# Optimization experiments

Measured on AMD Instinct MI355X. Metric: run time of the kernel, lower is better.

## Reference

```python
import jax, jax.numpy as jnp
import numpy as np

D_MODEL = 512; N_LAYERS = 6; D_STATE = 128; EXPAND = 2
D_INNER = EXPAND * D_MODEL          # 1024
HEADDIM = 64; NHEADS = D_INNER // HEADDIM  # 16
D_CONV = 4
CONV_DIM = D_INNER + 2 * D_STATE    # 1280 (x, B, C share the causal conv)
D_IN_PROJ = 2 * D_INNER + 2 * D_STATE + NHEADS  # 2320 (z, xBC, dt)
CHUNK = 128
B_SZ = 2; SEQ = 4096


def setup_inputs() -> dict:
    key = jax.random.key(0)
    ks = jax.random.split(key, 8)
    return {
        "x": jax.random.normal(ks[0], (B_SZ, SEQ, D_MODEL), jnp.float32),
        "in_proj_w": jax.random.normal(ks[1], (N_LAYERS, D_IN_PROJ, D_MODEL), jnp.float32) * 0.02,
        "conv_w": jax.random.normal(ks[2], (N_LAYERS, CONV_DIM, 1, D_CONV), jnp.float32) * 0.1,
        "conv_b": jnp.zeros((N_LAYERS, CONV_DIM), jnp.float32),
        "dt_bias": jax.random.normal(ks[3], (N_LAYERS, NHEADS), jnp.float32) * 0.5,
        "A_log": jnp.log(jax.random.uniform(ks[4], (N_LAYERS, NHEADS), jnp.float32, 1.0, 16.0)),
        "D": jax.random.normal(ks[5], (N_LAYERS, NHEADS), jnp.float32) * 0.1 + 1.0,
        "rms_w": jnp.ones((N_LAYERS, D_INNER), jnp.float32),
        "out_proj_w": jax.random.normal(ks[6], (N_LAYERS, D_MODEL, D_INNER), jnp.float32) * 0.02,
        "ln_w": jnp.ones((N_LAYERS, D_MODEL), jnp.float32),
        "ln_b": jnp.zeros((N_LAYERS, D_MODEL), jnp.float32),
        "fln_w": jnp.ones((D_MODEL,), jnp.float32),
        "fln_b": jnp.zeros((D_MODEL,), jnp.float32),
    }


def _layernorm(x, w, b, eps=1e-5):
    mu = jnp.mean(x, -1, keepdims=True)
    xc = x - mu
    var = jnp.mean(xc * xc, -1, keepdims=True)
    return xc * jax.lax.rsqrt(var + eps) * w + b


def _segsum(a):
    # a: (..., T) -> (..., T, T); S[i,j] = sum_{j<k<=i} a[k] for i>=j else -inf
    T = a.shape[-1]
    c = jnp.cumsum(a, -1)
    s = c[..., :, None] - c[..., None, :]
    return jnp.where(jnp.tril(jnp.ones((T, T), bool)), s, -jnp.inf)


def _ssd(xdt, Adt, Bm, Cm):
    # Chunked Mamba-2 SSD (math-identical to h_t = exp(dt*A) h_{t-1} + dt*B_t x_t; y_t = C_t h_t)
    # xdt: (b,l,h,p) = x*dt; Adt: (b,l,h) = dt*A; Bm, Cm: (b,l,n) (ngroups=1)
    b, l, h, p = xdt.shape
    n = Bm.shape[-1]
    c = l // CHUNK
    X = xdt.reshape(b, c, CHUNK, h, p)
    A = Adt.reshape(b, c, CHUNK, h).transpose(0, 3, 1, 2)  # (b,h,c,q)
    Bc = Bm.reshape(b, c, CHUNK, n)
    Cc = Cm.reshape(b, c, CHUNK, n)
    A_cs = jnp.cumsum(A, -1)                                # (b,h,c,q)
    Lm = jnp.exp(_segsum(A))                                # (b,h,c,q,q) intra-chunk decays
    Y_diag = jnp.einsum('bcqn,bcsn,bhcqs,bcshp->bcqhp', Cc, Bc, Lm, X)
    decay_states = jnp.exp(A_cs[..., -1:] - A_cs)           # (b,h,c,q)
    states = jnp.einsum('bcqn,bhcq,bcqhp->bchpn', Bc, decay_states, X)  # chunk end states
    A_last = A_cs[..., -1]                                  # (b,h,c)
    dc = jnp.exp(_segsum(jnp.pad(A_last, ((0, 0), (0, 0), (1, 0)))))    # (b,h,c+1,c+1)
    states = jnp.concatenate([jnp.zeros_like(states[:, :1]), states], axis=1)  # (b,c+1,h,p,n)
    new_states = jnp.einsum('bhzc,bchpn->bzhpn', dc, states)
    init_states = new_states[:, :-1]                        # state entering each chunk
    Y_off = jnp.einsum('bcqn,bchpn,bhcq->bcqhp', Cc, init_states, jnp.exp(A_cs))
    return (Y_diag + Y_off).reshape(b, l, h, p)


def _mamba2(u, Wi, cw, cb, dtb, Alog, Dh, rw, Wo):
    b, l, _ = u.shape
    zxbcdt = u @ Wi.T                                      # (b,l,2320)
    z = zxbcdt[..., :D_INNER]
    xBC = zxbcdt[..., D_INNER:D_INNER + CONV_DIM]
    dt = jax.nn.softplus(zxbcdt[..., D_INNER + CONV_DIM:] + dtb)  # (b,l,h)
    # causal depthwise conv (kernel 4)
    xp = jnp.pad(xBC, ((0, 0), (D_CONV - 1, 0), (0, 0))).transpose(0, 2, 1)
    conv = jax.lax.conv_general_dilated(xp, cw, (1,), 'VALID', feature_group_count=CONV_DIM)
    xBC = jax.nn.silu(conv.transpose(0, 2, 1) + cb)
    xh = xBC[..., :D_INNER].reshape(b, l, NHEADS, HEADDIM)
    Bm = xBC[..., D_INNER:D_INNER + D_STATE]
    Cm = xBC[..., D_INNER + D_STATE:]
    A = -jnp.exp(Alog)                                     # (h,)
    y = _ssd(xh * dt[..., None], dt * A, Bm, Cm)
    y = y + Dh[None, None, :, None] * xh                   # D skip
    y = y.reshape(b, l, D_INNER)
    yz = y * jax.nn.silu(z)                                # gated RMSNorm
    y = yz * jax.lax.rsqrt(jnp.mean(yz * yz, -1, keepdims=True) + 1e-5) * rw
    return y @ Wo.T


def reference(x, in_proj_w, conv_w, conv_b, dt_bias, A_log, D, rms_w, out_proj_w, ln_w, ln_b, fln_w, fln_b):
    h = x
    for i in range(N_LAYERS):
        res = h
        hn = _layernorm(h, ln_w[i], ln_b[i])
        h = _mamba2(hn, in_proj_w[i], conv_w[i], conv_b[i], dt_bias[i], A_log[i], D[i], rms_w[i], out_proj_w[i]) + res
    return _layernorm(h, fln_w, fln_b)
```

## Files before the change

### kernel.cpp

```cpp
#include <hip/hip_runtime.h>
#include <hip/hip_bf16.h>
#include <math.h>

#define BQ 2
#define SEQL 4096
#define DM 512
#define DIN 1024
#define DSTATE 128
#define NH 16
#define HD 64
#define DCONV 4
#define CONVDIM 1280
#define DINPROJ 2320
#define CHUNKL 128
#define NCHUNK 32
#define ROWS (BQ*SEQL)
#define NPAD 2304

typedef __attribute__((ext_vector_type(8))) short short8;
typedef __attribute__((ext_vector_type(4))) short short4v;
typedef __attribute__((ext_vector_type(4))) float f32x4;

__device__ __forceinline__ short bfs(float f) {
  __hip_bfloat16 h = __float2bfloat16(f);
  short s; __builtin_memcpy(&s, &h, 2); return s;
}
__device__ __forceinline__ float sbf(short s) {
  __hip_bfloat16 h; __builtin_memcpy(&h, &s, 2); return __bfloat162float(h);
}

__global__ __launch_bounds__(256) void ln_kernel(const float* __restrict__ in, const float* __restrict__ w,
                                                 const float* __restrict__ b, float* __restrict__ out,
                                                 __hip_bfloat16* __restrict__ outb) {
  int r = blockIdx.x;
  const float* x = in + (size_t)r * DM;
  float v[2];
  float s = 0.f, ss = 0.f;
  for (int i = 0; i < 2; i++) { v[i] = x[threadIdx.x + i*256]; s += v[i]; ss += v[i]*v[i]; }
  for (int o = 32; o > 0; o >>= 1) { s += __shfl_down(s, o); ss += __shfl_down(ss, o); }
  __shared__ float red[2][4];
  int lane = threadIdx.x & 63, wv = threadIdx.x >> 6;
  if (lane == 0) { red[0][wv] = s; red[1][wv] = ss; }
  __syncthreads();
  s  = red[0][0] + red[0][1] + red[0][2] + red[0][3];
  ss = red[1][0] + red[1][1] + red[1][2] + red[1][3];
  float mu = s * (1.f/DM);
  float var = ss * (1.f/DM) - mu*mu;
  float rstd = rsqrtf(var + 1e-5f);
  for (int i = 0; i < 2; i++) {
    int idx = threadIdx.x + i*256;
    float val = (v[i]-mu)*rstd*w[idx] + b[idx];
    out[(size_t)r*DM + idx] = val;
    if (outb) outb[(size_t)r*DM + idx] = __float2bfloat16(val);
  }
}

__global__ __launch_bounds__(256) void ln_dt_kernel(const float* __restrict__ in, const float* __restrict__ w,
                                                    const float* __restrict__ b, const float* __restrict__ Wi,
                                                    const float* __restrict__ dtb,
                                                    __hip_bfloat16* __restrict__ outb, float* __restrict__ dtout) {
  int r = blockIdx.x;
  const float* x = in + (size_t)r * DM;
  __shared__ float sh[512];
  __shared__ float red2[2][4];
  __shared__ float red[16][17];
  int t = threadIdx.x;
  float v[2];
  float s = 0.f, ss = 0.f;
  for (int i = 0; i < 2; i++) { v[i] = x[t + i*256]; s += v[i]; ss += v[i]*v[i]; }
  for (int o = 32; o > 0; o >>= 1) { s += __shfl_down(s, o); ss += __shfl_down(ss, o); }
  int lane = t & 63, wv = t >> 6;
  if (lane == 0) { red2[0][wv] = s; red2[1][wv] = ss; }
  __syncthreads();
  s  = red2[0][0] + red2[0][1] + red2[0][2] + red2[0][3];
  ss = red2[1][0] + red2[1][1] + red2[1][2] + red2[1][3];
  float mu = s * (1.f/DM);
  float var = ss * (1.f/DM) - mu*mu;
  float rstd = rsqrtf(var + 1e-5f);
  for (int i = 0; i < 2; i++) {
    int idx = t + i*256;
    float val = (v[i]-mu)*rstd*w[idx] + b[idx];
    sh[idx] = val;
    outb[(size_t)r*DM + idx] = __float2bfloat16(val);
  }
  __syncthreads();
  int j = t >> 4, seg = t & 15;
  const float* wrow = Wi + (size_t)(2304 + j)*DM + seg*32;
  float p = 0.f;
  #pragma unroll
  for (int k = 0; k < 32; k++) p += sh[seg*32 + k] * wrow[k];
  red[j][seg] = p;
  __syncthreads();
  if (t < 16) {
    float vv = 0.f;
    for (int sgi = 0; sgi < 16; sgi++) vv += red[t][sgi];
    vv += dtb[t];
    dtout[r*NH + t] = (vv > 20.f) ? vv : log1pf(__expf(vv));
  }
}

__global__ __launch_bounds__(256) void cvt_wi(const float* __restrict__ Wi, __hip_bfloat16* __restrict__ out) {
  int idx = blockIdx.x*256 + threadIdx.x;
  int l = idx / (NPAD*DM);
  int r = idx - l*(NPAD*DM);
  int n = r >> 9, k = r & 511;
  out[idx] = __float2bfloat16(Wi[(size_t)l*DINPROJ*DM + (size_t)n*DM + k]);
}
__global__ __launch_bounds__(256) void cvt_wo(const float* __restrict__ Wo, const float* __restrict__ rw,
                                              __hip_bfloat16* __restrict__ out) {
  size_t idx = (size_t)blockIdx.x*256 + threadIdx.x;
  int l = (int)(idx / (DM*DIN));
  int k = (int)(idx & (DIN-1));
  out[idx] = __float2bfloat16(Wo[idx] * rw[l*DIN + k]);
}

__global__ __launch_bounds__(256) void gemm_nt_obf16(const __hip_bfloat16* __restrict__ A,
                                                     const __hip_bfloat16* __restrict__ Bw,
                                                     __hip_bfloat16* __restrict__ C, int N, int K) {
  __shared__ __hip_bfloat16 sA[128*64];
  __shared__ __hip_bfloat16 sB[128*64];
  int tid = threadIdx.x;
  int w = tid >> 6, lane = tid & 63;
  int quad = lane >> 4, l16 = lane & 15;
  int nwg = gridDim.x * gridDim.y;
  int bid = blockIdx.x + blockIdx.y * gridDim.x;
  int qq = nwg >> 3;
  int bid2 = (bid & 7) * qq + (bid >> 3);
  int row0 = (bid2 / gridDim.x) * 128, col0 = (bid2 % gridDim.x) * 128;
  int srow = lane >> 3;
  int schunk = lane & 7;
  f32x4 acc[4][4];
  #pragma unroll
  for (int i = 0; i < 4; i++)
    #pragma unroll
    for (int j = 0; j < 4; j++) acc[i][j] = (f32x4){0.f,0.f,0.f,0.f};
  int wrow = (w >> 1) * 64, wcol = (w & 1) * 64;
  for (int k0 = 0; k0 < K; k0 += 64) {
    #pragma unroll
    for (int j = 0; j < 4; j++) {
      int r = w*32 + j*8 + srow;
      int gc = (schunk ^ (r & 7)) * 8;
      const __hip_bfloat16* ga = A + (size_t)(row0 + r)*K + k0 + gc;
      __builtin_amdgcn_global_load_lds((const __attribute__((address_space(1))) void*)ga,
          (__attribute__((address_space(3))) void*)(sA + (w*32 + j*8)*64), 16, 0, 0);
      const __hip_bfloat16* gb = Bw + (size_t)(col0 + r)*K + k0 + gc;
      __builtin_amdgcn_global_load_lds((const __attribute__((address_space(1))) void*)gb,
          (__attribute__((address_space(3))) void*)(sB + (w*32 + j*8)*64), 16, 0, 0);
    }
    __syncthreads();
    #pragma unroll
    for (int ks = 0; ks < 64; ks += 32) {
      short8 af[4], bfv[4];
      #pragma unroll
      for (int mt = 0; mt < 4; mt++) {
        int r = wrow + mt*16 + l16;
        int cch = (ks/8 + quad) ^ (r & 7);
        af[mt] = *(const short8*)(sA + r*64 + cch*8);
      }
      #pragma unroll
      for (int nt = 0; nt < 4; nt++) {
        int r = wcol + nt*16 + l16;
        int cch = (ks/8 + quad) ^ (r & 7);
        bfv[nt] = *(const short8*)(sB + r*64 + cch*8);
      }
      #pragma unroll
      for (int mt = 0; mt < 4; mt++)
        #pragma unroll
        for (int nt = 0; nt < 4; nt++)
          acc[mt][nt] = __builtin_amdgcn_mfma_f32_16x16x32_bf16(af[mt], bfv[nt], acc[mt][nt], 0, 0, 0);
    }
    __syncthreads();
  }
  #pragma unroll
  for (int mt = 0; mt < 4; mt++) {
    int r = row0 + wrow + mt*16 + quad*4;
    #pragma unroll
    for (int nt = 0; nt < 4; nt++) {
      int cidx = col0 + wcol + nt*16 + l16;
      if (cidx < N) {
        __hip_bfloat16* cp = C + (size_t)r*N + cidx;
        #pragma unroll
        for (int rg = 0; rg < 4; rg++)
          cp[(size_t)rg*N] = __float2bfloat16(acc[mt][nt][rg]);
      }
    }
  }
}

__global__ __launch_bounds__(256) void gemm_nt_addf32(const __hip_bfloat16* __restrict__ A,
                                                      const __hip_bfloat16* __restrict__ Bw,
                                                      const float* __restrict__ ssq,
                                                      float* __restrict__ C) {
  __shared__ __hip_bfloat16 sA[64*64];
  __shared__ __hip_bfloat16 sB[128*64];
  const int N = DM, K = DIN;
  int tid = threadIdx.x;
  int w = tid >> 6, lane = tid & 63;
  int quad = lane >> 4, l16 = lane & 15;
  int raw = blockIdx.x;
  int xcd = raw & 7, seq = raw >> 3;
  int panel = xcd*16 + (seq >> 2);
  int row0 = panel * 64;
  int col0 = (seq & 3) * 128;
  int srow = lane >> 3;
  int schunk = lane & 7;
  f32x4 acc[2][4];
  #pragma unroll
  for (int i = 0; i < 2; i++)
    #pragma unroll
    for (int j = 0; j < 4; j++) acc[i][j] = (f32x4){0.f,0.f,0.f,0.f};
  int wrow = (w >> 1) * 32, wcol = (w & 1) * 64;
  for (int k0 = 0; k0 < K; k0 += 64) {
    #pragma unroll
    for (int j = 0; j < 2; j++) {
      int r = w*16 + j*8 + srow;
      int gc = (schunk ^ (r & 7)) * 8;
      const __hip_bfloat16* ga = A + (size_t)(row0 + r)*K + k0 + gc;
      __builtin_amdgcn_global_load_lds((const __attribute__((address_space(1))) void*)ga,
          (__attribute__((address_space(3))) void*)(sA + (w*16 + j*8)*64), 16, 0, 0);
    }
    #pragma unroll
    for (int j = 0; j < 4; j++) {
      int r = w*32 + j*8 + srow;
      int gc = (schunk ^ (r & 7)) * 8;
      const __hip_bfloat16* gb = Bw + (size_t)(col0 + r)*K + k0 + gc;
      __builtin_amdgcn_global_load_lds((const __attribute__((address_space(1))) void*)gb,
          (__attribute__((address_space(3))) void*)(sB + (w*32 + j*8)*64), 16, 0, 0);
    }
    __syncthreads();
    #pragma unroll
    for (int ks = 0; ks < 64; ks += 32) {
      short8 af[2], bfv[4];
      #pragma unroll
      for (int mt = 0; mt < 2; mt++) {
        int r = wrow + mt*16 + l16;
        int cch = (ks/8 + quad) ^ (r & 7);
        af[mt] = *(const short8*)(sA + r*64 + cch*8);
      }
      #pragma unroll
      for (int nt = 0; nt < 4; nt++) {
        int r = wcol + nt*16 + l16;
        int cch = (ks/8 + quad) ^ (r & 7);
        bfv[nt] = *(const short8*)(sB + r*64 + cch*8);
      }
      #pragma unroll
      for (int mt = 0; mt < 2; mt++)
        #pragma unroll
        for (int nt = 0; nt < 4; nt++)
          acc[mt][nt] = __builtin_amdgcn_mfma_f32_16x16x32_bf16(af[mt], bfv[nt], acc[mt][nt], 0, 0, 0);
    }
    __syncthreads();
  }
  #pragma unroll
  for (int mt = 0; mt < 2; mt++) {
    int r = row0 + wrow + mt*16 + quad*4;
    float rsv[4];
    #pragma unroll
    for (int rg = 0; rg < 4; rg++)
      rsv[rg] = rsqrtf(ssq[r + rg]*(1.f/DIN) + 1e-5f);
    #pragma unroll
    for (int nt = 0; nt < 4; nt++) {
      int cidx = col0 + wcol + nt*16 + l16;
      float* cp = C + (size_t)r*N + cidx;
      #pragma unroll
      for (int rg = 0; rg < 4; rg++)
        cp[(size_t)rg*N] += rsv[rg]*acc[mt][nt][rg];
    }
  }
}

__global__ __launch_bounds__(256) void conv_tiled(const __hip_bfloat16* __restrict__ zx, const float* __restrict__ cw,
                                                  const float* __restrict__ cb, const float* __restrict__ dt,
                                                  __hip_bfloat16* __restrict__ bcb,
                                                  __hip_bfloat16* __restrict__ xtg, __hip_bfloat16* __restrict__ btg) {
  __shared__ float tile[35][260];
  int c0 = blockIdx.x * 256;
  int r0 = blockIdx.y * 32;
  int b = r0 >> 12, l0 = r0 & 4095;
  int t = threadIdx.x;
  for (int i = t; i < 35*64; i += 256) {
    int lr = i >> 6, c4 = (i & 63) * 4;
    int l = l0 - 3 + lr;
    float4 v = make_float4(0.f, 0.f, 0.f, 0.f);
    if (l >= 0) {
      short4v s = *(const short4v*)((const short*)zx + ((size_t)(b<<12) + l)*NPAD + 1024 + c0 + c4);
      v = make_float4(sbf(s[0]), sbf(s[1]), sbf(s[2]), sbf(s[3]));
    }
    *(float4*)&tile[lr][c4] = v;
  }
  __syncthreads();
  int c = c0 + t;
  float w0 = cw[c*4+0], w1 = cw[c*4+1], w2 = cw[c*4+2], w3 = cw[c*4+3];
  float bias = cb[c];
  float x0 = tile[0][t], x1 = tile[1][t], x2 = tile[2][t];
  if (c0 < DIN) {
    int h = c >> 6;
    const float* dtp = dt + (size_t)r0*NH + h;
    __hip_bfloat16* xo = xtg + ((size_t)(b*DIN + c))*SEQL + l0;
    for (int lb = 0; lb < 4; lb++) {
      short8 pk;
      #pragma unroll
      for (int jj = 0; jj < 8; jj++) {
        int l = lb*8 + jj;
        float x3 = tile[l+3][t];
        float acc = bias + w0*x0 + w1*x1 + w2*x2 + w3*x3;
        float sv = acc / (1.f + __expf(-acc));
        pk[jj] = bfs(sv * dtp[(size_t)l*NH]);
        x0 = x1; x1 = x2; x2 = x3;
      }
      *(short8*)(xo + lb*8) = pk;
    }
  } else {
    int n = c - DIN;
    __hip_bfloat16* bo = (n < DSTATE) ? (btg + ((size_t)(b*DSTATE + n))*SEQL + l0) : nullptr;
    for (int lb = 0; lb < 4; lb++) {
      short8 pk;
      #pragma unroll
      for (int jj = 0; jj < 8; jj++) {
        int l = lb*8 + jj;
        float x3 = tile[l+3][t];
        float acc = bias + w0*x0 + w1*x1 + w2*x2 + w3*x3;
        float sv = acc / (1.f + __expf(-acc));
        short bv = bfs(sv);
        bcb[(size_t)(r0 + l)*256 + n] = *(__hip_bfloat16*)&bv;
        pk[jj] = bv;
        x0 = x1; x1 = x2; x2 = x3;
      }
      if (bo) *(short8*)(bo + lb*8) = pk;
    }
  }
}

__global__ __launch_bounds__(512, 6) void ssd_states_mfma(const __hip_bfloat16* __restrict__ xtg,
                                                          const __hip_bfloat16* __restrict__ btg,
                                                          const float* __restrict__ dt,
                                                          const float* __restrict__ Alog,
                                                          float* __restrict__ states, float* __restrict__ acs_buf,
                                                          float* __restrict__ alast) {
  __shared__ short sBt[128][136];
  __shared__ short sXw[64][136];
  __shared__ float sa[128], sw[128];
  int raw = blockIdx.x;
  int bc = (raw & 7) + ((raw >> 7) << 3);
  int h = (raw >> 3) & 15;
  int b = bc >> 5, c = bc & 31;
  int sblk = bc*16 + h;
  int t = threadIdx.x;
  int w = t >> 6, lane = t & 63, quad = lane >> 4, l16 = lane & 15;
  size_t row0 = (size_t)(b*SEQL + c*CHUNKL);
  float Ah = -__expf(Alog[h]);
  if (t < 64) {
    float d0 = dt[(row0 + 2*t)*NH + h], d1 = dt[(row0 + 2*t + 1)*NH + h];
    float v0 = d0 * Ah, v1 = d1 * Ah;
    float s2 = v0 + v1;
    #pragma unroll
    for (int off = 1; off < 64; off <<= 1) {
      float tmp = __shfl_up(s2, off);
      if (t >= off) s2 += tmp;
    }
    float tot = __shfl(s2, 63);
    float pre = s2 - (v0 + v1);
    float a0 = pre + v0, a1 = pre + v0 + v1;
    sa[2*t] = a0; sa[2*t+1] = a1;
    sw[2*t] = __expf(tot - a0); sw[2*t+1] = __expf(tot - a1);
    acs_buf[(size_t)sblk*128 + 2*t]   = a0;
    acs_buf[(size_t)sblk*128 + 2*t+1] = a1;
    if (t == 63) alast[(b*NH + h)*NCHUNK + c] = tot;
  }
  __syncthreads();
  {
    const __hip_bfloat16* xb = xtg + ((size_t)(b*DIN + h*HD))*SEQL + c*CHUNKL;
    for (int i = t; i < 64*16; i += 512) {
      int p = i >> 4, q8 = (i & 15) * 8;
      short8 v = *(const short8*)(xb + (size_t)p*SEQL + q8);
      short8 o;
      #pragma unroll
      for (int j = 0; j < 8; j++) o[j] = bfs(sbf(v[j]) * sw[q8 + j]);
      *(short8*)&sXw[p][q8] = o;
    }
    const __hip_bfloat16* bb = btg + ((size_t)(b*DSTATE))*SEQL + c*CHUNKL;
    for (int i = t; i < 128*16; i += 512) {
      int n = i >> 4, q8 = (i & 15) * 8;
      *(short8*)&sBt[n][q8] = *(const short8*)(bb + (size_t)n*SEQL + q8);
    }
  }
  __syncthreads();
  int pt4 = w >> 1, nt4 = (w & 1) * 4;
  f32x4 st[4];
  #pragma unroll
  for (int j = 0; j < 4; j++) st[j] = (f32x4){0.f,0.f,0.f,0.f};
  #pragma unroll
  for (int ks = 0; ks < 128; ks += 32) {
    short8 af = *(const short8*)&sXw[pt4*16 + l16][ks + quad*8];
    #pragma unroll
    for (int j = 0; j < 4; j++) {
      short8 bfv = *(const short8*)&sBt[(nt4+j)*16 + l16][ks + quad*8];
      st[j] = __builtin_amdgcn_mfma_f32_16x16x32_bf16(af, bfv, st[j], 0, 0, 0);
    }
  }
  float* sp = states + (size_t)sblk*(HD*DSTATE);
  #pragma unroll
  for (int j = 0; j < 4; j++) {
    int n = (nt4+j)*16 + l16;
    #pragma unroll
    for (int rg = 0; rg < 4; rg++) {
      int p = pt4*16 + quad*4 + rg;
      sp[(size_t)p*DSTATE + n] = st[j][rg];
    }
  }
}

__global__ __launch_bounds__(256) void ssd_scan2(const float* __restrict__ states, const float* __restrict__ alast,
                                                 __hip_bfloat16* __restrict__ stb, float* __restrict__ ssq) {
  int idx = blockIdx.x*256 + threadIdx.x;
  if (idx < ROWS) ssq[idx] = 0.f;
  int b = idx >> 17;
  int h = (idx >> 13) & 15;
  int pn = idx & 8191;
  const float* al = alast + (b*NH + h)*NCHUNK;
  float S = 0.f;
  for (int c = 0; c < NCHUNK; c++) {
    size_t base = ((size_t)((b*NCHUNK + c)*NH + h))*8192 + pn;
    float dec = __expf(al[c]);
    float tmp = states[base];
    stb[base] = __float2bfloat16(S);
    S = dec*S + tmp;
  }
}

__global__ __launch_bounds__(1024, 4) void ssd_post_mfma(const __hip_bfloat16* __restrict__ bcb,
                                                         const __hip_bfloat16* __restrict__ xtg,
                                                         const float* __restrict__ dt,
                                                         const __hip_bfloat16* __restrict__ stb,
                                                         const float* __restrict__ acs_buf,
                                                         const float* __restrict__ Dvec,
                                                         const __hip_bfloat16* __restrict__ zx,
                                                         float* __restrict__ ssq,
                                                         __hip_bfloat16* __restrict__ Y) {
  __shared__ short sM[128][136];
  __shared__ short sXt[64][136];
  __shared__ short sS[64][136];
  __shared__ float sa[4][128];
  __shared__ float sdt4[4][128];
  __shared__ float ssrow[128];
  int raw = blockIdx.x;
  int xcd = raw & 7, slot = raw >> 3;
  int bc = xcd*8 + (slot >> 2);
  int hg = slot & 3;
  int b = bc >> 5, c = bc & 31;
  int t = threadIdx.x;
  int w = t >> 6, lane = t & 63, quad = lane >> 4, l16 = lane & 15;
  size_t row0 = (size_t)(b*SEQL + c*CHUNKL);
  const __hip_bfloat16* bcrow = bcb + row0*256;
  int mt = w >> 1, nt1 = (w & 1) * 4, pt3 = (w & 1) * 2;
  if (t < 128) ssrow[t] = 0.f;
  short8 af[4];
  #pragma unroll
  for (int k = 0; k < 4; k++)
    af[k] = *(const short8*)(bcrow + (size_t)(mt*16 + l16)*256 + 128 + k*32 + quad*8);
  for (int i = t; i < 128*16; i += 1024) {
    int q = i >> 4, n8 = (i & 15) * 8;
    *(short8*)&sM[q][n8] = *(const short8*)(bcrow + (size_t)q*256 + n8);
  }
  if (t < 512) {
    int hh = t >> 7, q = t & 127;
    int h = hg*4 + hh;
    sa[hh][q]   = acs_buf[(size_t)(bc*16 + h)*128 + q];
    sdt4[hh][q] = dt[(row0 + q)*NH + h];
  }
  {
    int h = hg*4;
    const __hip_bfloat16* xb = xtg + ((size_t)(b*DIN + h*HD))*SEQL + c*CHUNKL;
    int p = t >> 4, q8 = (t & 15) * 8;
    *(short8*)&sXt[p][q8] = *(const short8*)(xb + (size_t)p*SEQL + q8);
    const __hip_bfloat16* sbase = stb + (size_t)(bc*16 + h)*(HD*DSTATE);
    *(short8*)&sS[p][q8] = *(const short8*)(sbase + (size_t)p*DSTATE + q8);
  }
  __syncthreads();
  f32x4 g[4];
  #pragma unroll
  for (int j = 0; j < 4; j++) g[j] = (f32x4){0.f,0.f,0.f,0.f};
  #pragma unroll
  for (int ks = 0; ks < 4; ks++) {
    #pragma unroll
    for (int j = 0; j < 4; j++) {
      short8 bfv = *(const short8*)&sM[(nt1+j)*16 + l16][ks*32 + quad*8];
      g[j] = __builtin_amdgcn_mfma_f32_16x16x32_bf16(af[ks], bfv, g[j], 0, 0, 0);
    }
  }
  __syncthreads();
  for (int hh = 0; hh < 4; hh++) {
    int h = hg*4 + hh;
    #pragma unroll
    for (int j = 0; j < 4; j++) {
      int s = (nt1+j)*16 + l16;
      #pragma unroll
      for (int rg = 0; rg < 4; rg++) {
        int q = mt*16 + quad*4 + rg;
        float m = (s <= q) ? g[j][rg] * __expf(sa[hh][q] - sa[hh][s]) : 0.f;
        sM[q][s] = bfs(m);
      }
    }
    __syncthreads();
    f32x4 y4[2], yo[2];
    y4[0] = (f32x4){0.f,0.f,0.f,0.f}; y4[1] = (f32x4){0.f,0.f,0.f,0.f};
    yo[0] = (f32x4){0.f,0.f,0.f,0.f}; yo[1] = (f32x4){0.f,0.f,0.f,0.f};
    #pragma unroll
    for (int ks = 0; ks < 4; ks++) {
      short8 mf = *(const short8*)&sM[mt*16 + l16][ks*32 + quad*8];
      #pragma unroll
      for (int j = 0; j < 2; j++) {
        short8 xv = *(const short8*)&sXt[(pt3+j)*16 + l16][ks*32 + quad*8];
        y4[j] = __builtin_amdgcn_mfma_f32_16x16x32_bf16(mf, xv, y4[j], 0, 0, 0);
        short8 sv = *(const short8*)&sS[(pt3+j)*16 + l16][ks*32 + quad*8];
        yo[j] = __builtin_amdgcn_mfma_f32_16x16x32_bf16(af[ks], sv, yo[j], 0, 0, 0);
      }
    }
    float Dh = Dvec[h];
    float part[4];
    #pragma unroll
    for (int rg = 0; rg < 4; rg++) {
      int q = mt*16 + quad*4 + rg;
      float ea = __expf(sa[hh][q]);
      float drdt = Dh / sdt4[hh][q];
      float pr = 0.f;
      #pragma unroll
      for (int j = 0; j < 2; j++) {
        int p = (pt3+j)*16 + l16;
        int ch = h*HD + p;
        float yv = y4[j][rg] + ea*yo[j][rg] + drdt*sbf(sXt[p][q]);
        float z = sbf(*((const short*)zx + (row0+q)*NPAD + ch));
        float v = yv * z / (1.f + __expf(-z));
        Y[(row0 + q)*DIN + ch] = __float2bfloat16(v);
        pr += v*v;
      }
      part[rg] = pr;
    }
    #pragma unroll
    for (int rg = 0; rg < 4; rg++) {
      float pv = part[rg];
      #pragma unroll
      for (int off = 1; off < 16; off <<= 1) pv += __shfl_xor(pv, off);
      if (l16 == 0) atomicAdd(&ssrow[mt*16 + quad*4 + rg], pv);
    }
    __syncthreads();
    if (hh < 3) {
      int h2 = h + 1;
      const __hip_bfloat16* xb = xtg + ((size_t)(b*DIN + h2*HD))*SEQL + c*CHUNKL;
      int p = t >> 4, q8 = (t & 15) * 8;
      *(short8*)&sXt[p][q8] = *(const short8*)(xb + (size_t)p*SEQL + q8);
      const __hip_bfloat16* sbase = stb + (size_t)(bc*16 + h2)*(HD*DSTATE);
      *(short8*)&sS[p][q8] = *(const short8*)(sbase + (size_t)p*DSTATE + q8);
    }
  }
  if (t < 128) atomicAdd(&ssq[row0 + t], ssrow[t]);
}

extern "C" void kernel_launch(void* const* d_in, const int* in_sizes, int n_in,
                              void* d_out, int out_size, void* d_ws, size_t ws_size,
                              hipStream_t stream) {
  (void)in_sizes; (void)n_in; (void)out_size; (void)ws_size;
  const float* x    = (const float*)d_in[0];
  const float* Wi   = (const float*)d_in[1];
  const float* cw   = (const float*)d_in[2];
  const float* cb   = (const float*)d_in[3];
  const float* dtb  = (const float*)d_in[4];
  const float* Alog = (const float*)d_in[5];
  const float* Dv   = (const float*)d_in[6];
  const float* rw   = (const float*)d_in[7];
  const float* Wo   = (const float*)d_in[8];
  const float* lnw  = (const float*)d_in[9];
  const float* lnb  = (const float*)d_in[10];
  const float* flnw = (const float*)d_in[11];
  const float* flnb = (const float*)d_in[12];
  float* out = (float*)d_out;

  float* p = (float*)d_ws;
  float* buf_h   = p; p += (size_t)ROWS*DM;
  float* buf_dt  = p; p += (size_t)ROWS*NH;
  float* buf_st  = p; p += (size_t)BQ*NCHUNK*NH*HD*DSTATE;
  float* buf_acs = p; p += (size_t)BQ*NCHUNK*NH*CHUNKL;
  float* buf_al  = p; p += (size_t)BQ*NH*NCHUNK;
  float* buf_ssq = p; p += (size_t)ROWS;
  __hip_bfloat16* bp = (__hip_bfloat16*)p;
  __hip_bfloat16* buf_zx = bp; bp += (size_t)ROWS*NPAD;
  __hip_bfloat16* wi_b = bp; bp += (size_t)6*NPAD*DM;
  __hip_bfloat16* wo_b = bp; bp += (size_t)6*DM*DIN;
  __hip_bfloat16* hn_b = bp;
  __hip_bfloat16* Ybuf = bp; bp += (size_t)ROWS*DIN;
  __hip_bfloat16* bcb  = bp; bp += (size_t)ROWS*256;
  __hip_bfloat16* xtg  = bp; bp += (size_t)BQ*DIN*SEQL;
  __hip_bfloat16* btg  = bp; bp += (size_t)BQ*DSTATE*SEQL;
  __hip_bfloat16* stb  = bp; bp += (size_t)BQ*NCHUNK*NH*HD*DSTATE;

  hipMemcpyAsync(buf_h, x, (size_t)ROWS*DM*sizeof(float), hipMemcpyDeviceToDevice, stream);
  cvt_wi<<<6*NPAD*DM/256, 256, 0, stream>>>(Wi, wi_b);
  cvt_wo<<<6*DM*DIN/256, 256, 0, stream>>>(Wo, rw, wo_b);

  for (int i = 0; i < 6; i++) {
    ln_dt_kernel<<<ROWS, 256, 0, stream>>>(buf_h, lnw + i*DM, lnb + i*DM,
                                           Wi + (size_t)i*DINPROJ*DM, dtb + i*NH, hn_b, buf_dt);
    gemm_nt_obf16<<<dim3(NPAD/128, ROWS/128), 256, 0, stream>>>(
        hn_b, wi_b + (size_t)i*NPAD*DM, buf_zx, NPAD, DM);
    conv_tiled<<<dim3(CONVDIM/256, ROWS/32), 256, 0, stream>>>(
        buf_zx, cw + (size_t)i*CONVDIM*DCONV, cb + i*CONVDIM, buf_dt,
        bcb, xtg, btg);
    ssd_states_mfma<<<BQ*NCHUNK*NH, 512, 0, stream>>>(
        xtg, btg, buf_dt, Alog + i*NH, buf_st, buf_acs, buf_al);
    ssd_scan2<<<BQ*NH*HD*DSTATE/256, 256, 0, stream>>>(buf_st, buf_al, stb, buf_ssq);
    ssd_post_mfma<<<BQ*NCHUNK*4, 1024, 0, stream>>>(
        bcb, xtg, buf_dt, stb, buf_acs, Dv + i*NH, buf_zx, buf_ssq, Ybuf);
    gemm_nt_addf32<<<512, 256, 0, stream>>>(
        Ybuf, wo_b + (size_t)i*DM*DIN, buf_ssq, buf_h);
  }
  ln_kernel<<<ROWS, 256, 0, stream>>>(buf_h, flnw, flnb, out, nullptr);
}
```

Measured before the change: 1.073 ms.

## Store chunk states in bf16 in place and double-buffer per-head tiles in ssd_post

ssd_states_mfma now writes per-chunk states directly as bf16 into stb, and ssd_scan2 reads and overwrites that buffer in place, removing the fp32 states buffer and halving its read and write traffic. In ssd_post_mfma the X and state tiles are double-buffered in shared memory, so the next head's loads are issued before the current head's MFMAs rather than after the trailing sync. The cost is extra rounding, since states are quantized to bf16 before the scan accumulates them, and more LDS per block, which could limit occupancy of the 1024-thread blocks.

```diff
diff --git a/kernel.cpp b/kernel.cpp
--- a/kernel.cpp
+++ b/kernel.cpp
@@ -335,7 +335,8 @@
                                                           const __hip_bfloat16* __restrict__ btg,
                                                           const float* __restrict__ dt,
                                                           const float* __restrict__ Alog,
-                                                          float* __restrict__ states, float* __restrict__ acs_buf,
+                                                          __hip_bfloat16* __restrict__ stb,
+                                                          float* __restrict__ acs_buf,
                                                           float* __restrict__ alast) {
   __shared__ short sBt[128][136];
   __shared__ short sXw[64][136];
@@ -398,20 +399,20 @@
       st[j] = __builtin_amdgcn_mfma_f32_16x16x32_bf16(af, bfv, st[j], 0, 0, 0);
     }
   }
-  float* sp = states + (size_t)sblk*(HD*DSTATE);
+  __hip_bfloat16* sp = stb + (size_t)sblk*(HD*DSTATE);
   #pragma unroll
   for (int j = 0; j < 4; j++) {
     int n = (nt4+j)*16 + l16;
     #pragma unroll
     for (int rg = 0; rg < 4; rg++) {
       int p = pt4*16 + quad*4 + rg;
-      sp[(size_t)p*DSTATE + n] = st[j][rg];
-    }
-  }
-}
-
-__global__ __launch_bounds__(256) void ssd_scan2(const float* __restrict__ states, const float* __restrict__ alast,
-                                                 __hip_bfloat16* __restrict__ stb, float* __restrict__ ssq) {
+      sp[(size_t)p*DSTATE + n] = __float2bfloat16(st[j][rg]);
+    }
+  }
+}
+
+__global__ __launch_bounds__(256) void ssd_scan2(__hip_bfloat16* __restrict__ stb, const float* __restrict__ alast,
+                                                 float* __restrict__ ssq) {
   int idx = blockIdx.x*256 + threadIdx.x;
   if (idx < ROWS) ssq[idx] = 0.f;
   int b = idx >> 17;
@@ -422,7 +423,7 @@
   for (int c = 0; c < NCHUNK; c++) {
     size_t base = ((size_t)((b*NCHUNK + c)*NH + h))*8192 + pn;
     float dec = __expf(al[c]);
-    float tmp = states[base];
+    float tmp = __bfloat162float(stb[base]);
     stb[base] = __float2bfloat16(S);
     S = dec*S + tmp;
   }
@@ -438,8 +439,8 @@
                                                          float* __restrict__ ssq,
                                                          __hip_bfloat16* __restrict__ Y) {
   __shared__ short sM[128][136];
-  __shared__ short sXt[64][136];
-  __shared__ short sS[64][136];
+  __shared__ short sXt[2][64][136];
+  __shared__ short sS[2][64][136];
   __shared__ float sa[4][128];
   __shared__ float sdt4[4][128];
   __shared__ float ssrow[128];
@@ -472,9 +473,9 @@
     int h = hg*4;
     const __hip_bfloat16* xb = xtg + ((size_t)(b*DIN + h*HD))*SEQL + c*CHUNKL;
     int p = t >> 4, q8 = (t & 15) * 8;
-    *(short8*)&sXt[p][q8] = *(const short8*)(xb + (size_t)p*SEQL + q8);
+    *(short8*)&sXt[0][p][q8] = *(const short8*)(xb + (size_t)p*SEQL + q8);
     const __hip_bfloat16* sbase = stb + (size_t)(bc*16 + h)*(HD*DSTATE);
-    *(short8*)&sS[p][q8] = *(const short8*)(sbase + (size_t)p*DSTATE + q8);
+    *(short8*)&sS[0][p][q8] = *(const short8*)(sbase + (size_t)p*DSTATE + q8);
   }
   __syncthreads();
   f32x4 g[4];
@@ -491,6 +492,7 @@
   __syncthreads();
   for (int hh = 0; hh < 4; hh++) {
     int h = hg*4 + hh;
+    int cur = hh & 1;
     #pragma unroll
     for (int j = 0; j < 4; j++) {
       int s = (nt1+j)*16 + l16;
@@ -502,6 +504,14 @@
       }
     }
     __syncthreads();
+    if (hh < 3) {
+      int h2 = h + 1;
+      const __hip_bfloat16* xb = xtg + ((size_t)(b*DIN + h2*HD))*SEQL + c*CHUNKL;
+      int p = t >> 4, q8 = (t & 15) * 8;
+      *(short8*)&sXt[cur^1][p][q8] = *(const short8*)(xb + (size_t)p*SEQL + q8);
+      const __hip_bfloat16* sbase2 = stb + (size_t)(bc*16 + h2)*(HD*DSTATE);
+      *(short8*)&sS[cur^1][p][q8] = *(const short8*)(sbase2 + (size_t)p*DSTATE + q8);
+    }
     f32x4 y4[2], yo[2];
     y4[0] = (f32x4){0.f,0.f,0.f,0.f}; y4[1] = (f32x4){0.f,0.f,0.f,0.f};
     yo[0] = (f32x4){0.f,0.f,0.f,0.f}; yo[1] = (f32x4){0.f,0.f,0.f,0.f};
@@ -510,9 +520,9 @@
       short8 mf = *(const short8*)&sM[mt*16 + l16][ks*32 + quad*8];
       #pragma unroll
       for (int j = 0; j < 2; j++) {
-        short8 xv = *(const short8*)&sXt[(pt3+j)*16 + l16][ks*32 + quad*8];
+        short8 xv = *(const short8*)&sXt[cur][(pt3+j)*16 + l16][ks*32 + quad*8];
         y4[j] = __builtin_amdgcn_mfma_f32_16x16x32_bf16(mf, xv, y4[j], 0, 0, 0);
-        short8 sv = *(const short8*)&sS[(pt3+j)*16 + l16][ks*32 + quad*8];
+        short8 sv = *(const short8*)&sS[cur][(pt3+j)*16 + l16][ks*32 + quad*8];
         yo[j] = __builtin_amdgcn_mfma_f32_16x16x32_bf16(af[ks], sv, yo[j], 0, 0, 0);
       }
     }
@@ -528,7 +538,7 @@
       for (int j = 0; j < 2; j++) {
         int p = (pt3+j)*16 + l16;
         int ch = h*HD + p;
-        float yv = y4[j][rg] + ea*yo[j][rg] + drdt*sbf(sXt[p][q]);
+        float yv = y4[j][rg] + ea*yo[j][rg] + drdt*sbf(sXt[cur][p][q]);
         float z = sbf(*((const short*)zx + (row0+q)*NPAD + ch));
         float v = yv * z / (1.f + __expf(-z));
         Y[(row0 + q)*DIN + ch] = __float2bfloat16(v);
@@ -544,14 +554,6 @@
       if (l16 == 0) atomicAdd(&ssrow[mt*16 + quad*4 + rg], pv);
     }
     __syncthreads();
-    if (hh < 3) {
-      int h2 = h + 1;
-      const __hip_bfloat16* xb = xtg + ((size_t)(b*DIN + h2*HD))*SEQL + c*CHUNKL;
-      int p = t >> 4, q8 = (t & 15) * 8;
-      *(short8*)&sXt[p][q8] = *(const short8*)(xb + (size_t)p*SEQL + q8);
-      const __hip_bfloat16* sbase = stb + (size_t)(bc*16 + h2)*(HD*DSTATE);
-      *(short8*)&sS[p][q8] = *(const short8*)(sbase + (size_t)p*DSTATE + q8);
-    }
   }
   if (t < 128) atomicAdd(&ssq[row0 + t], ssrow[t]);
 }
@@ -578,7 +580,6 @@
   float* p = (float*)d_ws;
   float* buf_h   = p; p += (size_t)ROWS*DM;
   float* buf_dt  = p; p += (size_t)ROWS*NH;
-  float* buf_st  = p; p += (size_t)BQ*NCHUNK*NH*HD*DSTATE;
   float* buf_acs = p; p += (size_t)BQ*NCHUNK*NH*CHUNKL;
   float* buf_al  = p; p += (size_t)BQ*NH*NCHUNK;
   float* buf_ssq = p; p += (size_t)ROWS;
@@ -606,8 +607,8 @@
         buf_zx, cw + (size_t)i*CONVDIM*DCONV, cb + i*CONVDIM, buf_dt,
         bcb, xtg, btg);
     ssd_states_mfma<<<BQ*NCHUNK*NH, 512, 0, stream>>>(
-        xtg, btg, buf_dt, Alog + i*NH, buf_st, buf_acs, buf_al);
-    ssd_scan2<<<BQ*NH*HD*DSTATE/256, 256, 0, stream>>>(buf_st, buf_al, stb, buf_ssq);
+        xtg, btg, buf_dt, Alog + i*NH, stb, buf_acs, buf_al);
+    ssd_scan2<<<BQ*NH*HD*DSTATE/256, 256, 0, stream>>>(stb, buf_al, buf_ssq);
     ssd_post_mfma<<<BQ*NCHUNK*4, 1024, 0, stream>>>(
         bcb, xtg, buf_dt, stb, buf_acs, Dv + i*NH, buf_zx, buf_ssq, Ybuf);
     gemm_nt_addf32<<<512, 256, 0, stream>>>(
```

Result: faster. 1.013 ms, median of 3 (-5.6%).
